# Kernel tuning notes

Measured on AMD Instinct MI355X. Metric: run time of the kernel, lower is better.

The kernel has to match this reference:

```python
import jax, jax.numpy as jnp
import numpy as np

EPS = 1e-12  # torch F.normalize default eps


def setup_inputs() -> dict:
    key = jax.random.key(0)
    k1, k2, k3 = jax.random.split(key, 3)
    ns, d_in, n_feat, n_classes = 16384, 512, 256, 1000
    x = jax.random.normal(k1, (ns, d_in), dtype=jnp.float32)
    W = jax.random.normal(k2, (d_in, n_feat), dtype=jnp.float32) * 0.05
    # class prototypes: L2-normalized embeddings, one per seen class (seen_c == n_classes)
    means = jax.random.normal(k3, (n_classes, n_feat), dtype=jnp.float32)
    means = means / jnp.maximum(jnp.linalg.norm(means, axis=1, keepdims=True), EPS)
    return {"x": x, "W": W, "means": means, "t": 0}


def reference(x, W, means, t):
    # forward_training: backbone + L2 normalization along feature dim
    feats = x @ W                                   # [ns, n_feat]
    preds = feats / jnp.maximum(jnp.linalg.norm(feats, axis=1, keepdims=True), EPS)
    # deployment forward: nearest prototype by negative dot product
    # original: per-sample dist = -means @ pred^T; dist.min(0) -> class index
    dist = -(preds @ means.T)                       # [ns, seen_c]
    classpred = jnp.argmin(dist, axis=1)            # first min on ties, matches torch
    n_classes = means.shape[0]
    out = jax.nn.one_hot(classpred, n_classes, dtype=jnp.float32)  # [ns, n_classes]
    return out
```

## Files before the change

kernel.cpp:

```cpp
#include <hip/hip_runtime.h>
#include <float.h>

#define NS   16384
#define K1   512
#define F    256
#define NC   1000
#define SPB  64
#define NTHR 512
#define NBLK (NS / SPB)


typedef _Float16 half8  __attribute__((ext_vector_type(8)));
typedef _Float16 half4v __attribute__((ext_vector_type(4)));
typedef float    float4v __attribute__((ext_vector_type(4)));

#define M_OFF 262144

#define PREP_BLKS 192
#define ZERO_BLKS 2048

__global__ void prep(const float* __restrict__ W, const float* __restrict__ means,
                     _Float16* __restrict__ ws, float* __restrict__ out) {
    const int bid = blockIdx.x;
    if (bid >= PREP_BLKS) {
        const size_t total4 = (size_t)NS * NC / 4;
        const float4v z4 = (float4v){0.f, 0.f, 0.f, 0.f};
        size_t base = (size_t)(bid - PREP_BLKS) * 2048 + threadIdx.x;
#pragma unroll
        for (int j = 0; j < 8; ++j) {
            size_t q = base + (size_t)j * 256;
            if (q < total4)
                __builtin_nontemporal_store(
                    z4, reinterpret_cast<float4v*>(out) + q);
        }
        return;
    }
    int g = bid * blockDim.x + threadIdx.x;
    if (g < 16384) {
        int lane = g & 63, tile = g >> 6;
        int ks = tile >> 4, nt = tile & 15;
        int k0 = ks * 32 + (lane >> 4) * 8;
        int n  = nt * 16 + (lane & 15);
        half8 hv, lv;
#pragma unroll
        for (int j = 0; j < 8; ++j) {
            float v = W[(size_t)(k0 + j) * F + n] * 16.0f;
            _Float16 hi = (_Float16)v;
            hv[j] = hi;
            lv[j] = (_Float16)(v - (float)hi);
        }
        _Float16* d = ws + (size_t)tile * 1024 + (size_t)lane * 8;
        *reinterpret_cast<half8*>(d)       = hv;
        *reinterpret_cast<half8*>(d + 512) = lv;
    } else {
        int gm = g - 16384;
        int lane = gm & 63, tile = gm >> 6;
        int ks = tile >> 6, gt = tile & 63;
        int k0 = ks * 32 + (lane >> 4) * 8;
        int c  = gt * 16 + (lane & 15);
        half8 hv, lv;
#pragma unroll
        for (int j = 0; j < 8; ++j) {
            float v = (c < NC) ? means[(size_t)c * F + k0 + j] * 16.0f : 0.0f;
            _Float16 hi = (_Float16)v;
            hv[j] = hi;
            lv[j] = (_Float16)(v - (float)hi);
        }
        _Float16* d = ws + M_OFF + (size_t)tile * 1024 + (size_t)lane * 8;
        *reinterpret_cast<half8*>(d)       = hv;
        *reinterpret_cast<half8*>(d + 512) = lv;
    }
}

#define MFMA(a, b, c) __builtin_amdgcn_mfma_f32_16x16x32_f16((a), (b), (c), 0, 0, 0)

__attribute__((amdgpu_flat_work_group_size(NTHR, NTHR), amdgpu_waves_per_eu(2, 4)))
__global__ void fused_mfma(const float* __restrict__ x,
                           const _Float16* __restrict__ ws,
                           float* __restrict__ out) {
    __shared__ _Float16 xsh[2][64][40];
    __shared__ _Float16 xsl[2][64][40];
    __shared__ _Float16 fh[64][264];
    __shared__ _Float16 fl[64][264];
    __shared__ float cand_v[64][8];
    __shared__ int   cand_i[64][8];
    __shared__ int   bidx[64];

    const int tid  = threadIdx.x;
    const int lane = tid & 63;
    const int w    = tid >> 6;
    const int quad = lane >> 4;
    const int cl   = lane & 15;
    const int s0   = blockIdx.x * SPB;

    const int xrow = tid >> 3;
    const int xc4  = (tid & 7) * 4;

    float4v acc1[2][4];
#pragma unroll
    for (int p = 0; p < 2; ++p)
#pragma unroll
        for (int mt = 0; mt < 4; ++mt)
            acc1[p][mt] = (float4v){0.f, 0.f, 0.f, 0.f};

    const _Float16* wsrc = ws + ((size_t)(w * 2) << 10) + ((size_t)lane << 3);
    half8 wbh[2][2], wbl[2][2];
#pragma unroll
    for (int p = 0; p < 2; ++p) {
        wbh[0][p] = *reinterpret_cast<const half8*>(wsrc + p * 1024);
        wbl[0][p] = *reinterpret_cast<const half8*>(wsrc + p * 1024 + 512);
    }

    float4v xv = __builtin_nontemporal_load(
        reinterpret_cast<const float4v*>(x + (size_t)(s0 + xrow) * K1 + xc4));

#pragma unroll
    for (int ks = 0; ks < 16; ++ks) {
        const int buf = ks & 1;
        {
            half4v hx, lx;
#pragma unroll
            for (int j = 0; j < 4; ++j) {
                float v = xv[j] * 8.0f;
                _Float16 hi = (_Float16)v;
                hx[j] = hi;
                lx[j] = (_Float16)(v - (float)hi);
            }
            *reinterpret_cast<half4v*>(&xsh[buf][xrow][xc4]) = hx;
            *reinterpret_cast<half4v*>(&xsl[buf][xrow][xc4]) = lx;
        }
        __syncthreads();
        if (ks < 15)
            xv = __builtin_nontemporal_load(
                reinterpret_cast<const float4v*>(
                    x + (size_t)(s0 + xrow) * K1 + (ks + 1) * 32 + xc4));
        if (ks < 15) {
#pragma unroll
            for (int p = 0; p < 2; ++p) {
                wbh[buf ^ 1][p] = *reinterpret_cast<const half8*>(
                    wsrc + (size_t)(ks + 1) * 16384 + p * 1024);
                wbl[buf ^ 1][p] = *reinterpret_cast<const half8*>(
                    wsrc + (size_t)(ks + 1) * 16384 + p * 1024 + 512);
            }
        }
        half8 ah[4], al[4];
#pragma unroll
        for (int mt = 0; mt < 4; ++mt) {
            ah[mt] = *reinterpret_cast<const half8*>(&xsh[buf][mt * 16 + cl][quad * 8]);
            al[mt] = *reinterpret_cast<const half8*>(&xsl[buf][mt * 16 + cl][quad * 8]);
        }
#pragma unroll
        for (int p = 0; p < 2; ++p)
#pragma unroll
            for (int mt = 0; mt < 4; ++mt) {
                acc1[p][mt] = MFMA(ah[mt], wbh[buf][p], acc1[p][mt]);
                acc1[p][mt] = MFMA(ah[mt], wbl[buf][p], acc1[p][mt]);
                acc1[p][mt] = MFMA(al[mt], wbh[buf][p], acc1[p][mt]);
            }
    }

#pragma unroll
    for (int p = 0; p < 2; ++p)
#pragma unroll
        for (int mt = 0; mt < 4; ++mt)
#pragma unroll
            for (int r = 0; r < 4; ++r) {
                int srow = mt * 16 + quad * 4 + r;
                int n    = (w * 2 + p) * 16 + cl;
                float v  = acc1[p][mt][r];
                _Float16 hi = (_Float16)v;
                fh[srow][n] = hi;
                fl[srow][n] = (_Float16)(v - (float)hi);
            }
    __syncthreads();

    float4v acc2[4][8];
#pragma unroll
    for (int mt = 0; mt < 4; ++mt)
#pragma unroll
        for (int gt = 0; gt < 8; ++gt)
            acc2[mt][gt] = (float4v){0.f, 0.f, 0.f, 0.f};

    const _Float16* mbase = ws + M_OFF + ((size_t)(w * 8) << 10) + ((size_t)lane << 3);

    half8 mh[2], ml[2];
    mh[0] = *reinterpret_cast<const half8*>(mbase);
    ml[0] = *reinterpret_cast<const half8*>(mbase + 512);

#pragma unroll
    for (int ks = 0; ks < 8; ++ks) {
        half8 fah[4], fal[4];
#pragma unroll
        for (int mt = 0; mt < 4; ++mt) {
            fah[mt] = *reinterpret_cast<const half8*>(
                &fh[mt * 16 + cl][ks * 32 + quad * 8]);
            fal[mt] = *reinterpret_cast<const half8*>(
                &fl[mt * 16 + cl][ks * 32 + quad * 8]);
        }
#pragma unroll
        for (int gt = 0; gt < 8; ++gt) {
            const int ii = ks * 8 + gt;
            const int cb = ii & 1;
            if (ii < 63) {
                const _Float16* src = mbase +
                    (size_t)(((ii + 1) >> 3) * 65536 + ((ii + 1) & 7) * 1024);
                mh[cb ^ 1] = *reinterpret_cast<const half8*>(src);
                ml[cb ^ 1] = *reinterpret_cast<const half8*>(src + 512);
            }
#pragma unroll
            for (int mt = 0; mt < 4; ++mt) {
                acc2[mt][gt] = MFMA(fah[mt], mh[cb], acc2[mt][gt]);
                acc2[mt][gt] = MFMA(fah[mt], ml[cb], acc2[mt][gt]);
                acc2[mt][gt] = MFMA(fal[mt], mh[cb], acc2[mt][gt]);
            }
        }
    }

#pragma unroll
    for (int mt = 0; mt < 4; ++mt)
#pragma unroll
        for (int r = 0; r < 4; ++r) {
            float v  = -FLT_MAX;
            int   ix = 0x7FFFFFFF;
#pragma unroll
            for (int nt = 0; nt < 8; ++nt) {
                int c = (w * 8 + nt) * 16 + cl;
                if (c < NC) {
                    float sc = acc2[mt][nt][r];
                    if (sc > v) { v = sc; ix = c; }
                }
            }
#pragma unroll
            for (int off = 1; off < 16; off <<= 1) {
                float ov = __shfl_xor(v, off, 64);
                int   oi = __shfl_xor(ix, off, 64);
                if (ov > v || (ov == v && oi < ix)) { v = ov; ix = oi; }
            }
            if (cl == 0) {
                int srow = mt * 16 + quad * 4 + r;
                cand_v[srow][w] = v;
                cand_i[srow][w] = ix;
            }
        }
    __syncthreads();

    if (tid < SPB) {
        float v  = cand_v[tid][0];
        int   ix = cand_i[tid][0];
#pragma unroll
        for (int q = 1; q < 8; ++q) {
            float ov = cand_v[tid][q];
            int   oi = cand_i[tid][q];
            if (ov > v || (ov == v && oi < ix)) { v = ov; ix = oi; }
        }
        bidx[tid] = ix;
    }
    __syncthreads();

    if (tid < SPB)
        out[(size_t)(s0 + tid) * NC + bidx[tid]] = 1.0f;
}

extern "C" void kernel_launch(void* const* d_in, const int* in_sizes, int n_in,
                              void* d_out, int out_size, void* d_ws, size_t ws_size,
                              hipStream_t stream) {
    const float* x     = (const float*)d_in[0];
    const float* W     = (const float*)d_in[1];
    const float* means = (const float*)d_in[2];
    float* out         = (float*)d_out;
    _Float16* ws       = (_Float16*)d_ws;

    prep<<<PREP_BLKS + ZERO_BLKS, 256, 0, stream>>>(W, means, ws, out);
    fused_mfma<<<NBLK, NTHR, 0, stream>>>(x, ws, out);
}
```

Baseline: 141.3 us.

## Stream prototype tiles via global_load_lds FIFO with interleaved class assignment

The second GEMM now stages the fp16 hi/lo prototype tiles straight into a per-wave 4-slot LDS ring using global_load_lds, three tiles ahead, with explicit vmcnt waits. Before, each tile was loaded into registers and double-buffered. The ring reuses the LDS space of the x staging buffers, and class tiles are interleaved across waves (nt*8+w) rather than given to each wave as a contiguous block. The x loads also drop their nontemporal hint. The aim is deeper latency hiding and less register pressure for the prototype stream, at the cost of hand-managed waitcnt ordering that is fragile.

Result: faster. 135.3 us (-4.3%).

```diff
diff --git a/kernel.cpp b/kernel.cpp
--- a/kernel.cpp
+++ b/kernel.cpp
@@ -30,8 +30,7 @@
         for (int j = 0; j < 8; ++j) {
             size_t q = base + (size_t)j * 256;
             if (q < total4)
-                __builtin_nontemporal_store(
-                    z4, reinterpret_cast<float4v*>(out) + q);
+                __builtin_nontemporal_store(z4, reinterpret_cast<float4v*>(out) + q);
         }
         return;
     }
@@ -74,14 +73,26 @@
 
 #define MFMA(a, b, c) __builtin_amdgcn_mfma_f32_16x16x32_f16((a), (b), (c), 0, 0, 0)
 
+__device__ __forceinline__ void vmwait(int n) {
+    switch (n) {
+        case 0: asm volatile("s_waitcnt vmcnt(0)" ::: "memory"); break;
+        case 2: asm volatile("s_waitcnt vmcnt(2)" ::: "memory"); break;
+        case 4: asm volatile("s_waitcnt vmcnt(4)" ::: "memory"); break;
+        default: asm volatile("s_waitcnt vmcnt(6)" ::: "memory"); break;
+    }
+    __builtin_amdgcn_sched_barrier(0);
+}
+
+#define FH_OFF  0
+#define FL_OFF  16896
+#define OVL_OFF 33792
+#define SH_HALVES (33792 + 32768)
+
 __attribute__((amdgpu_flat_work_group_size(NTHR, NTHR), amdgpu_waves_per_eu(2, 4)))
 __global__ void fused_mfma(const float* __restrict__ x,
                            const _Float16* __restrict__ ws,
                            float* __restrict__ out) {
-    __shared__ _Float16 xsh[2][64][40];
-    __shared__ _Float16 xsl[2][64][40];
-    __shared__ _Float16 fh[64][264];
-    __shared__ _Float16 fl[64][264];
+    __shared__ _Float16 SH[SH_HALVES];
     __shared__ float cand_v[64][8];
     __shared__ int   cand_i[64][8];
     __shared__ int   bidx[64];
@@ -96,6 +107,11 @@
     const int xrow = tid >> 3;
     const int xc4  = (tid & 7) * 4;
 
+#define XSH(b,r,c) SH[OVL_OFF + (b)*2560 + (r)*40 + (c)]
+#define XSL(b,r,c) SH[OVL_OFF + 5120 + (b)*2560 + (r)*40 + (c)]
+#define FH(r,c)    SH[FH_OFF + (r)*264 + (c)]
+#define FL(r,c)    SH[FL_OFF + (r)*264 + (c)]
+
     float4v acc1[2][4];
 #pragma unroll
     for (int p = 0; p < 2; ++p)
@@ -111,8 +127,7 @@
         wbl[0][p] = *reinterpret_cast<const half8*>(wsrc + p * 1024 + 512);
     }
 
-    float4v xv = __builtin_nontemporal_load(
-        reinterpret_cast<const float4v*>(x + (size_t)(s0 + xrow) * K1 + xc4));
+    float4v xv = *reinterpret_cast<const float4v*>(x + (size_t)(s0 + xrow) * K1 + xc4);
 
 #pragma unroll
     for (int ks = 0; ks < 16; ++ks) {
@@ -126,14 +141,13 @@
                 hx[j] = hi;
                 lx[j] = (_Float16)(v - (float)hi);
             }
-            *reinterpret_cast<half4v*>(&xsh[buf][xrow][xc4]) = hx;
-            *reinterpret_cast<half4v*>(&xsl[buf][xrow][xc4]) = lx;
+            *reinterpret_cast<half4v*>(&XSH(buf, xrow, xc4)) = hx;
+            *reinterpret_cast<half4v*>(&XSL(buf, xrow, xc4)) = lx;
         }
         __syncthreads();
         if (ks < 15)
-            xv = __builtin_nontemporal_load(
-                reinterpret_cast<const float4v*>(
-                    x + (size_t)(s0 + xrow) * K1 + (ks + 1) * 32 + xc4));
+            xv = *reinterpret_cast<const float4v*>(
+                x + (size_t)(s0 + xrow) * K1 + (ks + 1) * 32 + xc4);
         if (ks < 15) {
 #pragma unroll
             for (int p = 0; p < 2; ++p) {
@@ -146,8 +160,8 @@
         half8 ah[4], al[4];
 #pragma unroll
         for (int mt = 0; mt < 4; ++mt) {
-            ah[mt] = *reinterpret_cast<const half8*>(&xsh[buf][mt * 16 + cl][quad * 8]);
-            al[mt] = *reinterpret_cast<const half8*>(&xsl[buf][mt * 16 + cl][quad * 8]);
+            ah[mt] = *reinterpret_cast<const half8*>(&XSH(buf, mt * 16 + cl, quad * 8));
+            al[mt] = *reinterpret_cast<const half8*>(&XSL(buf, mt * 16 + cl, quad * 8));
         }
 #pragma unroll
         for (int p = 0; p < 2; ++p)
@@ -169,8 +183,8 @@
                 int n    = (w * 2 + p) * 16 + cl;
                 float v  = acc1[p][mt][r];
                 _Float16 hi = (_Float16)v;
-                fh[srow][n] = hi;
-                fl[srow][n] = (_Float16)(v - (float)hi);
+                FH(srow, n) = hi;
+                FL(srow, n) = (_Float16)(v - (float)hi);
             }
     __syncthreads();
 
@@ -178,41 +192,60 @@
 #pragma unroll
     for (int mt = 0; mt < 4; ++mt)
 #pragma unroll
-        for (int gt = 0; gt < 8; ++gt)
-            acc2[mt][gt] = (float4v){0.f, 0.f, 0.f, 0.f};
-
-    const _Float16* mbase = ws + M_OFF + ((size_t)(w * 8) << 10) + ((size_t)lane << 3);
-
-    half8 mh[2], ml[2];
-    mh[0] = *reinterpret_cast<const half8*>(mbase);
-    ml[0] = *reinterpret_cast<const half8*>(mbase + 512);
-
-#pragma unroll
-    for (int ks = 0; ks < 8; ++ks) {
-        half8 fah[4], fal[4];
+        for (int c = 0; c < 8; ++c)
+            acc2[mt][c] = (float4v){0.f, 0.f, 0.f, 0.f};
+
+    _Float16* fifo = &SH[OVL_OFF + w * 4096];
+    const _Float16* mws = ws + M_OFF;
+
+#define MT_G(i) (mws + (size_t)((((i) >> 3) << 6) + (((i) & 7) << 3) + w) * 1024 \
+                     + (size_t)lane * 8)
+#define STAGE(i) do {                                                          \
+        const _Float16* g_ = MT_G(i);                                          \
+        _Float16* l_ = fifo + ((i) & 3) * 1024;                                \
+        __builtin_amdgcn_global_load_lds(                                      \
+            (const __attribute__((address_space(1))) void*)g_,                 \
+            (__attribute__((address_space(3))) void*)l_, 16, 0, 0);            \
+        __builtin_amdgcn_global_load_lds(                                      \
+            (const __attribute__((address_space(1))) void*)(g_ + 512),         \
+            (__attribute__((address_space(3))) void*)(l_ + 512), 16, 0, 0);    \
+    } while (0)
+
+    half8 fah[4], fal[4];
+    half8 fbh[2], fbl[2];
+
+    STAGE(0); STAGE(1); STAGE(2);
+    vmwait(4);
+    fbh[0] = *reinterpret_cast<const half8*>(fifo + lane * 8);
+    fbl[0] = *reinterpret_cast<const half8*>(fifo + 512 + lane * 8);
+
+#pragma unroll
+    for (int i = 0; i < 64; ++i) {
+        if (i < 61) STAGE(i + 3);
+        if (i < 61)      vmwait(4);
+        else if (i == 61) vmwait(2);
+        else if (i == 62) vmwait(0);
+        if (i < 63) {
+            const _Float16* sl = fifo + ((i + 1) & 3) * 1024 + lane * 8;
+            fbh[(i + 1) & 1] = *reinterpret_cast<const half8*>(sl);
+            fbl[(i + 1) & 1] = *reinterpret_cast<const half8*>(sl + 512);
+        }
+        if ((i & 7) == 0) {
+            const int ks = i >> 3;
+#pragma unroll
+            for (int mt = 0; mt < 4; ++mt) {
+                fah[mt] = *reinterpret_cast<const half8*>(
+                    &FH(mt * 16 + cl, ks * 32 + quad * 8));
+                fal[mt] = *reinterpret_cast<const half8*>(
+                    &FL(mt * 16 + cl, ks * 32 + quad * 8));
+            }
+        }
+        const int c = i & 7, rb = i & 1;
 #pragma unroll
         for (int mt = 0; mt < 4; ++mt) {
-            fah[mt] = *reinterpret_cast<const half8*>(
-                &fh[mt * 16 + cl][ks * 32 + quad * 8]);
-            fal[mt] = *reinterpret_cast<const half8*>(
-                &fl[mt * 16 + cl][ks * 32 + quad * 8]);
-        }
-#pragma unroll
-        for (int gt = 0; gt < 8; ++gt) {
-            const int ii = ks * 8 + gt;
-            const int cb = ii & 1;
-            if (ii < 63) {
-                const _Float16* src = mbase +
-                    (size_t)(((ii + 1) >> 3) * 65536 + ((ii + 1) & 7) * 1024);
-                mh[cb ^ 1] = *reinterpret_cast<const half8*>(src);
-                ml[cb ^ 1] = *reinterpret_cast<const half8*>(src + 512);
-            }
-#pragma unroll
-            for (int mt = 0; mt < 4; ++mt) {
-                acc2[mt][gt] = MFMA(fah[mt], mh[cb], acc2[mt][gt]);
-                acc2[mt][gt] = MFMA(fah[mt], ml[cb], acc2[mt][gt]);
-                acc2[mt][gt] = MFMA(fal[mt], mh[cb], acc2[mt][gt]);
-            }
+            acc2[mt][c] = MFMA(fah[mt], fbh[rb], acc2[mt][c]);
+            acc2[mt][c] = MFMA(fah[mt], fbl[rb], acc2[mt][c]);
+            acc2[mt][c] = MFMA(fal[mt], fbh[rb], acc2[mt][c]);
         }
     }
 
@@ -224,7 +257,7 @@
             int   ix = 0x7FFFFFFF;
 #pragma unroll
             for (int nt = 0; nt < 8; ++nt) {
-                int c = (w * 8 + nt) * 16 + cl;
+                int c = (nt * 8 + w) * 16 + cl;
                 if (c < NC) {
                     float sc = acc2[mt][nt][r];
                     if (sc > v) { v = sc; ix = c; }
```
